# Kernel optimization log

Measured on AMD Instinct MI355X. Metric: run time of the kernel, lower is better.

The kernel has to match this reference:

```python
import jax, jax.numpy as jnp
import numpy as np

H, DR, DN = 16, 64, 64
HD = DR + DN  # 128
EPS = 1e-6


def _ln(t):
    m = t.mean(-1, keepdims=True)
    v = ((t - m) ** 2).mean(-1, keepdims=True)
    return (t - m) / jnp.sqrt(v + EPS)


def _rms(t, w):
    return t * jax.lax.rsqrt((t * t).mean(-1, keepdims=True) + EPS) * w


def _rot(t, fcs):
    # t: [b,s,h,DR]; fcs: [s, DR//2, 2] (cos,sin); complex multiply on pairs
    b, s, h, d = t.shape
    tr = t.reshape(b, s, h, d // 2, 2)
    x0, x1 = tr[..., 0], tr[..., 1]
    cos = fcs[None, :, None, :, 0]
    sin = fcs[None, :, None, :, 1]
    o0 = x0 * cos - x1 * sin
    o1 = x0 * sin + x1 * cos
    return jnp.stack([o0, o1], axis=-1).reshape(b, s, h, d)


def setup_inputs() -> dict:
    key = jax.random.key(0)
    ks = jax.random.split(key, 12)
    B, SX, SY, D = 1, 2048, 512, 2048
    s = 0.02
    pos_x = jnp.arange(SX, dtype=jnp.float32)
    pos_y = jnp.arange(SY, dtype=jnp.float32)
    inv = 1.0 / (10000.0 ** (jnp.arange(0, DR, 2, dtype=jnp.float32) / DR))  # [32]
    ang_x = pos_x[:, None] * inv[None, :]
    ang_y = pos_y[:, None] * inv[None, :]
    return {
        "x": jax.random.normal(ks[0], (B, SX, D), jnp.float32),
        "y": jax.random.normal(ks[1], (B, SY, D), jnp.float32),
        "mod": jax.random.normal(ks[2], (B, D), jnp.float32),
        "freqs_x": jnp.stack([jnp.cos(ang_x), jnp.sin(ang_x)], -1),
        "freqs_y": jnp.stack([jnp.cos(ang_y), jnp.sin(ang_y)], -1),
        "mask_x": jnp.ones((B, SX), bool),
        "mask_y": jnp.ones((B, SY), bool),
        "Wqkv_x": jax.random.normal(ks[3], (HD * H * 3, D), jnp.float32) * s,
        "bqkv_x": jnp.zeros((HD * H * 3,), jnp.float32),
        "Wqkv_y": jax.random.normal(ks[4], (HD * H * 3, D), jnp.float32) * s,
        "bqkv_y": jnp.zeros((HD * H * 3,), jnp.float32),
        "Wout": jax.random.normal(ks[5], (D, HD * H), jnp.float32) * s,
        "bout": jnp.zeros((D,), jnp.float32),
        "wq": jnp.ones((HD,), jnp.float32),
        "wk": jnp.ones((HD,), jnp.float32),
        "Wmod_q": jax.random.normal(ks[6], (D * 3, D), jnp.float32) * s,
        "bmod_q": jnp.zeros((D * 3,), jnp.float32),
        "Wmod_kv": jax.random.normal(ks[7], (D * 3, D), jnp.float32) * s,
        "bmod_kv": jnp.zeros((D * 3,), jnp.float32),
    }


def reference(x, y, mod, freqs_x, freqs_y, mask_x, mask_y, Wqkv_x, bqkv_x,
              Wqkv_y, bqkv_y, Wout, bout, wq, wk, Wmod_q, bmod_q, Wmod_kv, bmod_kv):
    b, sx, D = x.shape
    sy = y.shape[1]
    sz = sx + sy
    x_res, y_res = x, y
    xn = _ln(x)
    yn = _ln(y)
    # modulation from mod vector [b, D] -> [b, 1, 3D]
    mq = mod[:, None, :] @ Wmod_q.T + bmod_q
    bias_x, scale_x, gate_x = jnp.split(mq, 3, axis=-1)
    mkv = mod[:, None, :] @ Wmod_kv.T + bmod_kv
    bias_y, scale_y, gate_y = jnp.split(mkv, 3, axis=-1)
    xm = (1.0 + scale_x) * xn + bias_x
    ym = (1.0 + scale_y) * yn + bias_y
    qx, kx, vx = jnp.split(xm @ Wqkv_x.T + bqkv_x, 3, axis=-1)
    qy, ky, vy = jnp.split(ym @ Wqkv_y.T + bqkv_y, 3, axis=-1)
    q = jnp.concatenate([qx, qy], 1).reshape(b, sz, H, HD)
    k = jnp.concatenate([kx, ky], 1).reshape(b, sz, H, HD)
    v = jnp.concatenate([vx, vy], 1).reshape(b, sz, H, HD)
    q = _rms(q, wq)
    k = _rms(k, wk)
    q_rope, q_nope = q[..., :DR], q[..., DR:]
    k_rope, k_nope = k[..., :DR], k[..., DR:]
    fxx = jnp.concatenate([freqs_x, jnp.zeros_like(freqs_y)], 0)
    fyy = jnp.concatenate([jnp.zeros_like(freqs_x), freqs_y], 0)
    qf = jnp.concatenate([_rot(q_rope, fxx), _rot(q_rope, fyy), q_nope], -1)
    kf = jnp.concatenate([_rot(k_rope, fxx), _rot(k_rope, fyy), k_nope], -1)
    d_attn = 2 * DR + DN  # 192
    scale = 1.0 / jnp.sqrt(jnp.float32(d_attn))
    scores = jnp.einsum('bshd,bthd->bhst', qf, kf) * scale
    mask = jnp.concatenate([mask_x, mask_y], 1)  # [b, sz] bool, key-side
    scores = jnp.where(mask[:, None, None, :], scores, -jnp.inf)
    attn = jax.nn.softmax(scores, axis=-1)
    z = jnp.einsum('bhst,bthd->bshd', attn, v).reshape(b, sz, H * HD)
    z = z @ Wout.T + bout
    xo = z[:, :sx] * gate_x + x_res
    yo = z[:, sx:] * gate_y + y_res
    return jnp.concatenate([xo, yo], axis=1)  # [b, sz, D]
```

## Files before the change

### kernel.cpp

```cpp
#include <hip/hip_runtime.h>
#include <math.h>

#define H_    16
#define DR_   64
#define HD_   128
#define D_    2048
#define SX_   2048
#define SY_   512
#define SZ_   2560
#define NQKV_ 6144
#define EPS_  1e-6f
#define ATTN_SCALE 0.07216878364870323f
#define NS_   4
#define SPL_  (SZ_ / NS_)
#define QT_   (SZ_ / 128)

typedef __attribute__((ext_vector_type(8)))  short short8;
typedef __attribute__((ext_vector_type(16))) float f32x16;

__device__ __forceinline__ unsigned short f2bf(float f) {
    unsigned u = __builtin_bit_cast(unsigned, f);
    u += 0x7FFF + ((u >> 16) & 1);
    return (unsigned short)(u >> 16);
}
__device__ __forceinline__ unsigned pack2(float a, float b) {
    return (unsigned)f2bf(a) | ((unsigned)f2bf(b) << 16);
}
__device__ __forceinline__ float bf2f_lo(unsigned u) {
    return __builtin_bit_cast(float, u << 16);
}
__device__ __forceinline__ float bf2f_hi(unsigned u) {
    return __builtin_bit_cast(float, u & 0xffff0000u);
}

__device__ __forceinline__ unsigned cvtpk_bf16(float lo, float hi) {
    unsigned r;
    asm volatile("v_cvt_pk_bf16_f32 %0, %1, %2" : "=v"(r) : "v"(lo), "v"(hi));
    return r;
}

__device__ __forceinline__ void gload16(const unsigned short* g, unsigned short* l) {
    __builtin_amdgcn_global_load_lds(
        (const __attribute__((address_space(1))) unsigned*)g,
        (__attribute__((address_space(3))) unsigned*)l, 16, 0, 0);
}

__device__ __forceinline__ int xcd_swz(int hw, int nwg) {
    return (hw & 7) * (nwg >> 3) + (hw >> 3);
}

__device__ __forceinline__ short8 mkfrag(const float* p) {
    unsigned a01 = cvtpk_bf16(p[0], p[1]);
    unsigned a23 = cvtpk_bf16(p[2], p[3]);
    unsigned a45 = cvtpk_bf16(p[4], p[5]);
    unsigned a67 = cvtpk_bf16(p[6], p[7]);
    asm volatile("v_permlane32_swap_b32 %0, %1" : "+v"(a01), "+v"(a45));
    asm volatile("v_permlane32_swap_b32 %0, %1" : "+v"(a23), "+v"(a67));
    union { unsigned u[4]; short8 s; } r;
    r.u[0] = a01; r.u[1] = a23; r.u[2] = a45; r.u[3] = a67;
    return r.s;
}

__global__ __launch_bounds__(256) void cvt_all_kernel(
    const float* __restrict__ s1, const float* __restrict__ s2, const float* __restrict__ s3,
    unsigned short* __restrict__ dst, int n1, int n2, int n3)
{
    int i = (blockIdx.x * 256 + threadIdx.x) * 8;
    if (i >= n1 + n2 + n3) return;
    const float* src;
    if (i < n1)            src = s1 + i;
    else if (i < n1 + n2)  src = s2 + (i - n1);
    else                   src = s3 + (i - n1 - n2);
    float4 a = *(const float4*)(src);
    float4 b = *(const float4*)(src + 4);
    uint4 pk;
    pk.x = pack2(a.x, a.y); pk.y = pack2(a.z, a.w);
    pk.z = pack2(b.x, b.y); pk.w = pack2(b.z, b.w);
    *(uint4*)(dst + i) = pk;
}

__global__ __launch_bounds__(256) void mod_gemv_kernel(
    const float* __restrict__ mod,
    const float* __restrict__ Wq, const float* __restrict__ bq,
    const float* __restrict__ Wkv, const float* __restrict__ bkv,
    float* __restrict__ mq, float* __restrict__ mkv)
{
    int t = threadIdx.x;
    int row = blockIdx.x * 4 + (t >> 6);
    int lane = t & 63;
    const float* W; const float* b; float* out; int r;
    if (row < NQKV_) { W = Wq;  b = bq;  out = mq;  r = row; }
    else             { W = Wkv; b = bkv; out = mkv; r = row - NQKV_; }
    const float* wr = W + (size_t)r * D_;
    float s = 0.f;
    for (int k = lane; k < D_; k += 64) s += wr[k] * mod[k];
#pragma unroll
    for (int m = 32; m >= 1; m >>= 1) s += __shfl_xor(s, m);
    if (lane == 0) out[r] = s + b[r];
}

__global__ __launch_bounds__(256) void ln_mod_kernel(
    const float* __restrict__ x, const float* __restrict__ y,
    const float* __restrict__ mq, const float* __restrict__ mkv,
    unsigned short* __restrict__ xm)
{
    __shared__ float red[8];
    int s = blockIdx.x, t = threadIdx.x;
    const float* src; const float* mv;
    if (s < SX_) { src = x + (size_t)s * D_;          mv = mq; }
    else         { src = y + (size_t)(s - SX_) * D_;  mv = mkv; }
    float a[8];
    *(float4*)&a[0] = *(const float4*)(src + t * 8);
    *(float4*)&a[4] = *(const float4*)(src + t * 8 + 4);
    float sum = 0.f, ssq = 0.f;
#pragma unroll
    for (int i = 0; i < 8; ++i) { sum += a[i]; ssq += a[i] * a[i]; }
#pragma unroll
    for (int m = 32; m >= 1; m >>= 1) { sum += __shfl_xor(sum, m); ssq += __shfl_xor(ssq, m); }
    if ((t & 63) == 0) { red[t >> 6] = sum; red[4 + (t >> 6)] = ssq; }
    __syncthreads();
    float tot  = red[0] + red[1] + red[2] + red[3];
    float totq = red[4] + red[5] + red[6] + red[7];
    float mean = tot * (1.f / (float)D_);
    float var  = totq * (1.f / (float)D_) - mean * mean;
    float inv  = rsqrtf(var + EPS_);
    float o[8];
#pragma unroll
    for (int i = 0; i < 8; ++i) {
        int c = t * 8 + i;
        float v = (a[i] - mean) * inv;
        o[i] = (1.f + mv[D_ + c]) * v + mv[c];
    }
    uint4 pk;
    pk.x = pack2(o[0], o[1]); pk.y = pack2(o[2], o[3]);
    pk.z = pack2(o[4], o[5]); pk.w = pack2(o[6], o[7]);
    *(uint4*)(xm + (size_t)s * D_ + t * 8) = pk;
}

__global__ __launch_bounds__(256) void gemm_bf16_kernel(
    const unsigned short* __restrict__ A,
    const unsigned short* __restrict__ Wx, const float* __restrict__ bx,
    const unsigned short* __restrict__ Wy, const float* __restrict__ by,
    void* __restrict__ Cout, int N,
    const float* __restrict__ gx, const float* __restrict__ gy,
    const float* __restrict__ rx, const float* __restrict__ ry,
    int mode)
{
    __shared__ __align__(16) unsigned short As[2][128 * 32];
    __shared__ __align__(16) unsigned short Bs[2][128 * 32];
    int m0 = blockIdx.y * 128, n0 = blockIdx.x * 128;
    const unsigned short* W = (m0 < SX_) ? Wx : Wy;
    const float* bb = (m0 < SX_) ? bx : by;
    int t = threadIdx.x;
    int wv = t >> 6, lane = t & 63, l31 = lane & 31, g = lane >> 5;
    int wr = wv >> 1, wc = wv & 1;
    int srow = t >> 2, ssl = t & 3;
    const unsigned short* gA = A + (size_t)(m0 + srow) * D_ + ((ssl ^ ((srow >> 1) & 3)) * 8);
    const unsigned short* gW = W + (size_t)(n0 + srow) * D_ + ((ssl ^ ((srow >> 1) & 3)) * 8);
    f32x16 acc[2][2];
#pragma unroll
    for (int i = 0; i < 2; ++i)
#pragma unroll
        for (int j = 0; j < 2; ++j)
#pragma unroll
            for (int r = 0; r < 16; ++r) acc[i][j][r] = 0.f;
    int arow = wr * 64 + l31;
    int wrow = wc * 64 + l31;
    int a3 = (arow >> 1) & 3, w3 = (wrow >> 1) & 3;

    gload16(gA,            &As[0][wv * 512]);
    gload16(gA + 64 * D_,  &As[0][2048 + wv * 512]);
    gload16(gW,            &Bs[0][wv * 512]);
    gload16(gW + 64 * D_,  &Bs[0][2048 + wv * 512]);
    __syncthreads();

    for (int k0 = 0; k0 < D_; k0 += 32) {
        int cur = (k0 >> 5) & 1;
        if (k0 + 32 < D_) {
            int nb = cur ^ 1;
            gload16(gA + k0 + 32,           &As[nb][wv * 512]);
            gload16(gA + 64 * D_ + k0 + 32, &As[nb][2048 + wv * 512]);
            gload16(gW + k0 + 32,           &Bs[nb][wv * 512]);
            gload16(gW + 64 * D_ + k0 + 32, &Bs[nb][2048 + wv * 512]);
        }
#pragma unroll
        for (int kk = 0; kk < 2; ++kk) {
            int slot = kk * 2 + g;
            short8 af[2], wf[2];
#pragma unroll
            for (int i = 0; i < 2; ++i) {
                af[i] = *(const short8*)&As[cur][(arow + i * 32) * 32 + ((slot ^ a3) * 8)];
                wf[i] = *(const short8*)&Bs[cur][(wrow + i * 32) * 32 + ((slot ^ w3) * 8)];
            }
#pragma unroll
            for (int i = 0; i < 2; ++i)
#pragma unroll
                for (int j = 0; j < 2; ++j)
                    acc[i][j] = __builtin_amdgcn_mfma_f32_32x32x16_bf16(wf[j], af[i], acc[i][j], 0, 0, 0);
        }
        __syncthreads();
    }

#pragma unroll
    for (int i = 0; i < 2; ++i) {
        int row = m0 + wr * 64 + i * 32 + l31;
        if (mode == 0) {
            unsigned short* C = (unsigned short*)Cout;
#pragma unroll
            for (int j = 0; j < 2; ++j)
#pragma unroll
                for (int q = 0; q < 4; ++q) {
                    int n = n0 + wc * 64 + j * 32 + q * 8 + 4 * g;
                    float o0 = acc[i][j][q * 4 + 0] + bb[n + 0];
                    float o1 = acc[i][j][q * 4 + 1] + bb[n + 1];
                    float o2 = acc[i][j][q * 4 + 2] + bb[n + 2];
                    float o3 = acc[i][j][q * 4 + 3] + bb[n + 3];
                    *(uint2*)(C + (size_t)row * N + n) = make_uint2(pack2(o0, o1), pack2(o2, o3));
                }
        } else {
            float* C = (float*)Cout;
            const float* gt = (row < SX_) ? gx : gy;
            const float* rr = (row < SX_) ? rx + (size_t)row * N : ry + (size_t)(row - SX_) * N;
#pragma unroll
            for (int j = 0; j < 2; ++j)
#pragma unroll
                for (int q = 0; q < 4; ++q) {
                    int n = n0 + wc * 64 + j * 32 + q * 8 + 4 * g;
                    float4 o;
                    o.x = (acc[i][j][q * 4 + 0] + bb[n + 0]) * gt[n + 0] + rr[n + 0];
                    o.y = (acc[i][j][q * 4 + 1] + bb[n + 1]) * gt[n + 1] + rr[n + 1];
                    o.z = (acc[i][j][q * 4 + 2] + bb[n + 2]) * gt[n + 2] + rr[n + 2];
                    o.w = (acc[i][j][q * 4 + 3] + bb[n + 3]) * gt[n + 3] + rr[n + 3];
                    *(float4*)(C + (size_t)row * N + n) = o;
                }
        }
    }
}

__global__ __launch_bounds__(256) void qkv_transform_kernel(
    const unsigned short* __restrict__ qkv,
    const float* __restrict__ fx, const float* __restrict__ fy,
    const float* __restrict__ wq, const float* __restrict__ wk,
    unsigned short* __restrict__ qh, unsigned short* __restrict__ kh,
    unsigned short* __restrict__ vh)
{
    int t = threadIdx.x;
    int gid = blockIdx.x * 4 + (t >> 6);
    int lane = t & 63;
    int s = gid >> 4;
    int h = gid & 15;
    const unsigned short* base = qkv + (size_t)s * NQKV_ + h * HD_;
    int d = lane * 2;
    unsigned qu = *(const unsigned*)(base + d);
    unsigned ku = *(const unsigned*)(base + 2048 + d);
    unsigned vu = *(const unsigned*)(base + 4096 + d);
    float qx = bf2f_lo(qu), qy = bf2f_hi(qu);
    float kx = bf2f_lo(ku), ky = bf2f_hi(ku);
    float sq = qx * qx + qy * qy;
    float sk = kx * kx + ky * ky;
#pragma unroll
    for (int m = 32; m >= 1; m >>= 1) { sq += __shfl_xor(sq, m); sk += __shfl_xor(sk, m); }
    float qs = rsqrtf(sq * (1.f / 128.f) + EPS_) * ATTN_SCALE;
    float ks = rsqrtf(sk * (1.f / 128.f) + EPS_);
    float q0 = qx * qs * wq[d], q1 = qy * qs * wq[d + 1];
    float k0 = kx * ks * wk[d], k1 = ky * ks * wk[d + 1];
    if (lane < 32) {
        const float* f = (s < SX_) ? fx + (size_t)s * DR_ + d
                                   : fy + (size_t)(s - SX_) * DR_ + d;
        float cs = f[0], sn = f[1];
        float o0 = q0 * cs - q1 * sn, o1 = q0 * sn + q1 * cs;
        q0 = o0; q1 = o1;
        o0 = k0 * cs - k1 * sn; o1 = k0 * sn + k1 * cs;
        k0 = o0; k1 = o1;
    }
    size_t off = ((size_t)h * SZ_ + s) * HD_ + d;
    *(unsigned*)(qh + off) = pack2(q0, q1);
    *(unsigned*)(kh + off) = pack2(k0, k1);
    *(unsigned*)(vh + off) = vu;
}

__global__ __launch_bounds__(256) void vtrans_kernel(
    const unsigned short* __restrict__ vh, unsigned short* __restrict__ vt)
{
    __shared__ __align__(16) unsigned short T[64][72];
    int h = blockIdx.z, d0 = blockIdx.y * 64, s0 = blockIdx.x * 64;
    int t = threadIdx.x;
    int r = t >> 2, c = (t & 3) * 16;
    const unsigned short* src = vh + ((size_t)h * SZ_ + s0 + r) * HD_ + d0 + c;
    *(short8*)&T[r][c]     = *(const short8*)(src);
    *(short8*)&T[r][c + 8] = *(const short8*)(src + 8);
    __syncthreads();
    unsigned short o16[16];
#pragma unroll
    for (int i = 0; i < 16; ++i) o16[i] = T[c + i][r];
    unsigned short* dst = vt + ((size_t)h * HD_ + d0 + r) * SZ_ + s0 + c;
    *(short8*)dst       = *(short8*)&o16[0];
    *(short8*)(dst + 8) = *(short8*)&o16[8];
}

__global__ __launch_bounds__(256) void attn_mfma_kernel(
    const unsigned short* __restrict__ qh, const unsigned short* __restrict__ kh,
    const unsigned short* __restrict__ vt,
    unsigned short* __restrict__ Opart, float* __restrict__ mpart, float* __restrict__ lpart)
{
    __shared__ __align__(16) short Ks[2][64 * 128];
    __shared__ __align__(16) short Vs[2][128 * 64];
    int hw = (blockIdx.z * gridDim.y + blockIdx.y) * gridDim.x + blockIdx.x;
    int lg = xcd_swz(hw, QT_ * H_ * NS_);
    int qt    = lg % QT_;
    int hs    = lg / QT_;
    int h     = hs % H_;
    int split = hs / H_;
    int t = threadIdx.x;
    int wv = t >> 6, lane = t & 63;
    int l31 = lane & 31, g = lane >> 5;
    int bq = qt * 128 + wv * 32;
    const unsigned short* kbase = kh + (size_t)h * SZ_ * HD_;
    const unsigned short* vbase = vt + (size_t)h * HD_ * SZ_;

    int koff[4], voff[4];
#pragma unroll
    for (int i = 0; i < 4; ++i) {
        int idx = i * 256 + t;
        int r = idx >> 4, sl = idx & 15;
        koff[i] = r * HD_ + (((sl & 8) | ((sl ^ (r & 7)) & 7)) * 8);
        int r2 = idx >> 3, sl2 = idx & 7;
        voff[i] = r2 * SZ_ + ((sl2 ^ (r2 & 7)) * 8);
    }
    int ldsOff = wv * 512;

    short8 qf[8];
    {
        const unsigned short* qb = qh + ((size_t)h * SZ_ + bq + l31) * HD_ + g * 8;
#pragma unroll
        for (int s = 0; s < 8; ++s) qf[s] = *(const short8*)(qb + s * 16);
    }

    f32x16 o[4];
#pragma unroll
    for (int db = 0; db < 4; ++db)
#pragma unroll
        for (int r = 0; r < 16; ++r) o[db][r] = 0.f;
    float mreg = -INFINITY, lreg = 0.f;
    bool qY = (bq >= SX_);
    int sw7 = l31 & 7;
    int ts0 = split * SPL_;
    const int NT = SPL_ / 64;

#pragma unroll
    for (int i = 0; i < 4; ++i)
        gload16(kbase + (size_t)ts0 * HD_ + koff[i], (unsigned short*)&Ks[0][0] + i * 2048 + ldsOff);
#pragma unroll
    for (int i = 0; i < 4; ++i)
        gload16(vbase + ts0 + voff[i], (unsigned short*)&Vs[0][0] + i * 2048 + ldsOff);
    __syncthreads();

    for (int it = 0; it < NT; ++it) {
        int t0 = ts0 + it * 64;
        int cur = it & 1;
        if (it + 1 < NT) {
            int nb = cur ^ 1;
            const unsigned short* kn = kbase + (size_t)(t0 + 64) * HD_;
            const unsigned short* vn = vbase + (t0 + 64);
#pragma unroll
            for (int i = 0; i < 4; ++i)
                gload16(kn + koff[i], (unsigned short*)&Ks[nb][0] + i * 2048 + ldsOff);
#pragma unroll
            for (int i = 0; i < 4; ++i)
                gload16(vn + voff[i], (unsigned short*)&Vs[nb][0] + i * 2048 + ldsOff);
        }

        bool same = (qY == (t0 >= SX_));
        f32x16 sc0, sc1;
#pragma unroll
        for (int r = 0; r < 16; ++r) { sc0[r] = 0.f; sc1[r] = 0.f; }
        const short* Krow0 = &Ks[cur][0] + l31 * 128;
        const short* Krow1 = &Ks[cur][0] + (l31 + 32) * 128;
        __builtin_amdgcn_s_setprio(1);
#pragma unroll
        for (int s = 4; s < 8; ++s) {
            int slot = 2 * s + g;
            int sl = (slot & 8) | ((slot ^ sw7) & 7);
            sc0 = __builtin_amdgcn_mfma_f32_32x32x16_bf16(*(const short8*)(Krow0 + sl * 8), qf[s], sc0, 0, 0, 0);
            sc1 = __builtin_amdgcn_mfma_f32_32x32x16_bf16(*(const short8*)(Krow1 + sl * 8), qf[s], sc1, 0, 0, 0);
        }
        if (same) {
#pragma unroll
            for (int s = 0; s < 4; ++s) {
                int slot = 2 * s + g;
                int sl = (slot & 8) | ((slot ^ sw7) & 7);
                sc0 = __builtin_amdgcn_mfma_f32_32x32x16_bf16(*(const short8*)(Krow0 + sl * 8), qf[s], sc0, 0, 0, 0);
                sc1 = __builtin_amdgcn_mfma_f32_32x32x16_bf16(*(const short8*)(Krow1 + sl * 8), qf[s], sc1, 0, 0, 0);
            }
        }
        __builtin_amdgcn_s_setprio(0);

        float pm = -INFINITY;
#pragma unroll
        for (int r = 0; r < 16; ++r) pm = fmaxf(pm, fmaxf(sc0[r], sc1[r]));
        pm = fmaxf(pm, __shfl_xor(pm, 32));
        float mnew = fmaxf(mreg, pm);
        float corr = __expf(mreg - mnew);
        mreg = mnew;
        float pp0[16], pp1[16]; float rs = 0.f;
#pragma unroll
        for (int r = 0; r < 16; ++r) {
            pp0[r] = __expf(sc0[r] - mnew);
            pp1[r] = __expf(sc1[r] - mnew);
            rs += pp0[r] + pp1[r];
        }
        rs += __shfl_xor(rs, 32);
        lreg = lreg * corr + rs;
#pragma unroll
        for (int db = 0; db < 4; ++db)
#pragma unroll
            for (int r = 0; r < 16; ++r) o[db][r] *= corr;

        short8 pa0 = mkfrag(&pp0[0]), pa1 = mkfrag(&pp0[8]);
        short8 pa2 = mkfrag(&pp1[0]), pa3 = mkfrag(&pp1[8]);
        const short* Vb = &Vs[cur][0];
        __builtin_amdgcn_s_setprio(1);
#pragma unroll
        for (int ks = 0; ks < 4; ++ks) {
            short8 pf = (ks == 0) ? pa0 : (ks == 1) ? pa1 : (ks == 2) ? pa2 : pa3;
#pragma unroll
            for (int db = 0; db < 4; ++db) {
                int row = db * 32 + l31;
                int sl = (2 * ks + g) ^ (l31 & 7);
                const short8 vf = *(const short8*)(Vb + row * 64 + sl * 8);
                o[db] = __builtin_amdgcn_mfma_f32_32x32x16_bf16(vf, pf, o[db], 0, 0, 0);
            }
        }
        __builtin_amdgcn_s_setprio(0);
        __syncthreads();
    }

    int basep = ((split * QT_ + qt) * H_ + h) * 128 + wv * 32 + l31;
    unsigned short* op = Opart + (size_t)basep * 128;
#pragma unroll
    for (int db = 0; db < 4; ++db)
#pragma unroll
        for (int r = 0; r < 16; ++r) {
            int d = db * 32 + (r & 3) + 8 * (r >> 2) + 4 * g;
            op[d] = f2bf(o[db][r]);
        }
    if (g == 0) { mpart[basep] = mreg; lpart[basep] = lreg; }
}

__global__ __launch_bounds__(256) void attn_combine_kernel(
    const unsigned short* __restrict__ Opart,
    const float* __restrict__ mpart, const float* __restrict__ lpart,
    unsigned short* __restrict__ z)
{
    int t = threadIdx.x;
    int gid = blockIdx.x * 4 + (t >> 6);
    int lane = t & 63;
    int h = gid & 15;
    int r = gid >> 4;
    int qtile = r >> 7, qi = r & 127;
    int pidx[NS_];
    float m[NS_];
    float mx = -INFINITY;
#pragma unroll
    for (int s = 0; s < NS_; ++s) {
        pidx[s] = ((s * QT_ + qtile) * H_ + h) * 128 + qi;
        m[s] = mpart[pidx[s]];
        mx = fmaxf(mx, m[s]);
    }
    float L = 0.f;
    float w[NS_];
#pragma unroll
    for (int s = 0; s < NS_; ++s) {
        w[s] = __expf(m[s] - mx);
        L += w[s] * lpart[pidx[s]];
    }
    float invL = 1.f / L;
    int d = lane * 2;
    float a0 = 0.f, a1 = 0.f;
#pragma unroll
    for (int s = 0; s < NS_; ++s) {
        unsigned u = *(const unsigned*)(Opart + (size_t)pidx[s] * 128 + d);
        a0 += w[s] * bf2f_lo(u);
        a1 += w[s] * bf2f_hi(u);
    }
    *(unsigned*)(z + (size_t)r * D_ + h * HD_ + d) = pack2(a0 * invL, a1 * invL);
}

extern "C" void kernel_launch(void* const* d_in, const int* in_sizes, int n_in,
                              void* d_out, int out_size, void* d_ws, size_t ws_size,
                              hipStream_t stream) {
    const float* x    = (const float*)d_in[0];
    const float* y    = (const float*)d_in[1];
    const float* mod  = (const float*)d_in[2];
    const float* fx   = (const float*)d_in[3];
    const float* fy   = (const float*)d_in[4];
    const float* Wqx  = (const float*)d_in[7];
    const float* bqx  = (const float*)d_in[8];
    const float* Wqy  = (const float*)d_in[9];
    const float* bqy  = (const float*)d_in[10];
    const float* Wout = (const float*)d_in[11];
    const float* bout = (const float*)d_in[12];
    const float* wq   = (const float*)d_in[13];
    const float* wk   = (const float*)d_in[14];
    const float* Wmq  = (const float*)d_in[15];
    const float* bmq  = (const float*)d_in[16];
    const float* Wmk  = (const float*)d_in[17];
    const float* bmk  = (const float*)d_in[18];

    float* mq   = (float*)d_ws;
    float* mkv  = mq + NQKV_;
    unsigned short* xm   = (unsigned short*)(mkv + NQKV_);
    unsigned short* qkvb = xm + (size_t)SZ_ * D_;
    unsigned short* qh   = qkvb + (size_t)SZ_ * NQKV_;
    unsigned short* kh   = qh + (size_t)H_ * SZ_ * HD_;
    unsigned short* vh   = kh + (size_t)H_ * SZ_ * HD_;
    unsigned short* vt   = vh + (size_t)H_ * SZ_ * HD_;
    unsigned short* wqxb = vt + (size_t)H_ * SZ_ * HD_;
    unsigned short* wqyb = wqxb + (size_t)NQKV_ * D_;
    unsigned short* wob  = wqyb + (size_t)NQKV_ * D_;
    unsigned short* z    = xm;
    unsigned short* Opart = wqxb;
    float* mpart = (float*)qkvb;
    float* lpart = mpart + NS_ * QT_ * H_ * 128;
    float* out  = (float*)d_out;

    const int n1 = NQKV_ * D_, n3 = D_ * D_;
    hipLaunchKernelGGL(cvt_all_kernel, dim3((2 * n1 + n3) / 2048), dim3(256), 0, stream,
                       Wqx, Wqy, Wout, wqxb, n1, n1, n3);
    hipLaunchKernelGGL(mod_gemv_kernel, dim3(2 * NQKV_ / 4), dim3(256), 0, stream,
                       mod, Wmq, bmq, Wmk, bmk, mq, mkv);
    hipLaunchKernelGGL(ln_mod_kernel, dim3(SZ_), dim3(256), 0, stream,
                       x, y, mq, mkv, xm);
    hipLaunchKernelGGL(gemm_bf16_kernel, dim3(NQKV_ / 128, SZ_ / 128), dim3(256), 0, stream,
                       xm, wqxb, bqx, wqyb, bqy, (void*)qkvb, NQKV_,
                       (const float*)nullptr, (const float*)nullptr,
                       (const float*)nullptr, (const float*)nullptr, 0);
    hipLaunchKernelGGL(qkv_transform_kernel, dim3(SZ_ * H_ / 4), dim3(256), 0, stream,
                       qkvb, fx, fy, wq, wk, qh, kh, vh);
    hipLaunchKernelGGL(vtrans_kernel, dim3(SZ_ / 64, HD_ / 64, H_), dim3(256), 0, stream,
                       vh, vt);
    hipLaunchKernelGGL(attn_mfma_kernel, dim3(QT_, H_, NS_), dim3(256), 0, stream,
                       qh, kh, vt, Opart, mpart, lpart);
    hipLaunchKernelGGL(attn_combine_kernel, dim3(SZ_ * H_ / 4), dim3(256), 0, stream,
                       Opart, mpart, lpart, z);
    hipLaunchKernelGGL(gemm_bf16_kernel, dim3(D_ / 128, SZ_ / 128), dim3(256), 0, stream,
                       z, wob, bout, wob, bout, (void*)out, D_,
                       mq + 2 * D_, mkv + 2 * D_, x, y, 1);
}
```

Before: 343.8 us.

## Deepen GEMM pipeline to two k-stages per barrier; read V directly from QKV buffer

The bf16 GEMM now uses four LDS buffers and processes two 32-wide k-slices per iteration. It loads the next pair while computing the current pair, with a single vmcnt wait and barrier per 64 k. This halves the number of barriers and gives the loads more time to overlap with MFMA work, at the cost of doubling LDS use per block, which may lower occupancy. Separately, the V head-major intermediate copy is removed and the transpose kernel reads V straight from the QKV GEMM output, saving one write and one read pass.

```diff
diff --git a/kernel.cpp b/kernel.cpp
--- a/kernel.cpp
+++ b/kernel.cpp
@@ -146,8 +146,8 @@
     const float* __restrict__ rx, const float* __restrict__ ry,
     int mode)
 {
-    __shared__ __align__(16) unsigned short As[2][128 * 32];
-    __shared__ __align__(16) unsigned short Bs[2][128 * 32];
+    __shared__ __align__(16) unsigned short As[4][128 * 32];
+    __shared__ __align__(16) unsigned short Bs[4][128 * 32];
     int m0 = blockIdx.y * 128, n0 = blockIdx.x * 128;
     const unsigned short* W = (m0 < SX_) ? Wx : Wy;
     const float* bb = (m0 < SX_) ? bx : by;
@@ -168,37 +168,49 @@
     int wrow = wc * 64 + l31;
     int a3 = (arow >> 1) & 3, w3 = (wrow >> 1) & 3;
 
-    gload16(gA,            &As[0][wv * 512]);
-    gload16(gA + 64 * D_,  &As[0][2048 + wv * 512]);
-    gload16(gW,            &Bs[0][wv * 512]);
-    gload16(gW + 64 * D_,  &Bs[0][2048 + wv * 512]);
-    __syncthreads();
-
-    for (int k0 = 0; k0 < D_; k0 += 32) {
-        int cur = (k0 >> 5) & 1;
-        if (k0 + 32 < D_) {
-            int nb = cur ^ 1;
-            gload16(gA + k0 + 32,           &As[nb][wv * 512]);
-            gload16(gA + 64 * D_ + k0 + 32, &As[nb][2048 + wv * 512]);
-            gload16(gW + k0 + 32,           &Bs[nb][wv * 512]);
-            gload16(gW + 64 * D_ + k0 + 32, &Bs[nb][2048 + wv * 512]);
-        }
-#pragma unroll
-        for (int kk = 0; kk < 2; ++kk) {
-            int slot = kk * 2 + g;
-            short8 af[2], wf[2];
-#pragma unroll
-            for (int i = 0; i < 2; ++i) {
-                af[i] = *(const short8*)&As[cur][(arow + i * 32) * 32 + ((slot ^ a3) * 8)];
-                wf[i] = *(const short8*)&Bs[cur][(wrow + i * 32) * 32 + ((slot ^ w3) * 8)];
+#pragma unroll
+    for (int s = 0; s < 2; ++s) {
+        gload16(gA + s * 32,           &As[s][wv * 512]);
+        gload16(gA + 64 * D_ + s * 32, &As[s][2048 + wv * 512]);
+        gload16(gW + s * 32,           &Bs[s][wv * 512]);
+        gload16(gW + 64 * D_ + s * 32, &Bs[s][2048 + wv * 512]);
+    }
+
+    const int NIT = D_ / 64;
+    for (int it = 0; it < NIT; ++it) {
+        int rb = (it & 1) * 2;
+        asm volatile("s_waitcnt vmcnt(0)" ::: "memory");
+        __builtin_amdgcn_s_barrier();
+        if (it + 1 < NIT) {
+            int k2 = (2 * it + 2) * 32;
+            int pb = 2 - rb;
+#pragma unroll
+            for (int s = 0; s < 2; ++s) {
+                gload16(gA + k2 + s * 32,           &As[pb + s][wv * 512]);
+                gload16(gA + 64 * D_ + k2 + s * 32, &As[pb + s][2048 + wv * 512]);
+                gload16(gW + k2 + s * 32,           &Bs[pb + s][wv * 512]);
+                gload16(gW + 64 * D_ + k2 + s * 32, &Bs[pb + s][2048 + wv * 512]);
             }
-#pragma unroll
-            for (int i = 0; i < 2; ++i)
-#pragma unroll
-                for (int j = 0; j < 2; ++j)
-                    acc[i][j] = __builtin_amdgcn_mfma_f32_32x32x16_bf16(wf[j], af[i], acc[i][j], 0, 0, 0);
-        }
-        __syncthreads();
+        }
+#pragma unroll
+        for (int s = 0; s < 2; ++s) {
+            int cur = rb + s;
+#pragma unroll
+            for (int kk = 0; kk < 2; ++kk) {
+                int slot = kk * 2 + g;
+                short8 af[2], wf[2];
+#pragma unroll
+                for (int i = 0; i < 2; ++i) {
+                    af[i] = *(const short8*)&As[cur][(arow + i * 32) * 32 + ((slot ^ a3) * 8)];
+                    wf[i] = *(const short8*)&Bs[cur][(wrow + i * 32) * 32 + ((slot ^ w3) * 8)];
+                }
+#pragma unroll
+                for (int i = 0; i < 2; ++i)
+#pragma unroll
+                    for (int j = 0; j < 2; ++j)
+                        acc[i][j] = __builtin_amdgcn_mfma_f32_32x32x16_bf16(wf[j], af[i], acc[i][j], 0, 0, 0);
+            }
+        }
     }
 
 #pragma unroll
@@ -241,8 +253,7 @@
     const unsigned short* __restrict__ qkv,
     const float* __restrict__ fx, const float* __restrict__ fy,
     const float* __restrict__ wq, const float* __restrict__ wk,
-    unsigned short* __restrict__ qh, unsigned short* __restrict__ kh,
-    unsigned short* __restrict__ vh)
+    unsigned short* __restrict__ qh, unsigned short* __restrict__ kh)
 {
     int t = threadIdx.x;
     int gid = blockIdx.x * 4 + (t >> 6);
@@ -253,7 +264,6 @@
     int d = lane * 2;
     unsigned qu = *(const unsigned*)(base + d);
     unsigned ku = *(const unsigned*)(base + 2048 + d);
-    unsigned vu = *(const unsigned*)(base + 4096 + d);
     float qx = bf2f_lo(qu), qy = bf2f_hi(qu);
     float kx = bf2f_lo(ku), ky = bf2f_hi(ku);
     float sq = qx * qx + qy * qy;
@@ -276,17 +286,16 @@
     size_t off = ((size_t)h * SZ_ + s) * HD_ + d;
     *(unsigned*)(qh + off) = pack2(q0, q1);
     *(unsigned*)(kh + off) = pack2(k0, k1);
-    *(unsigned*)(vh + off) = vu;
 }
 
 __global__ __launch_bounds__(256) void vtrans_kernel(
-    const unsigned short* __restrict__ vh, unsigned short* __restrict__ vt)
+    const unsigned short* __restrict__ qkvb, unsigned short* __restrict__ vt)
 {
     __shared__ __align__(16) unsigned short T[64][72];
     int h = blockIdx.z, d0 = blockIdx.y * 64, s0 = blockIdx.x * 64;
     int t = threadIdx.x;
     int r = t >> 2, c = (t & 3) * 16;
-    const unsigned short* src = vh + ((size_t)h * SZ_ + s0 + r) * HD_ + d0 + c;
+    const unsigned short* src = qkvb + (size_t)(s0 + r) * NQKV_ + 4096 + h * HD_ + d0 + c;
     *(short8*)&T[r][c]     = *(const short8*)(src);
     *(short8*)&T[r][c + 8] = *(const short8*)(src + 8);
     __syncthreads();
@@ -536,9 +545,9 @@
                        (const float*)nullptr, (const float*)nullptr,
                        (const float*)nullptr, (const float*)nullptr, 0);
     hipLaunchKernelGGL(qkv_transform_kernel, dim3(SZ_ * H_ / 4), dim3(256), 0, stream,
-                       qkvb, fx, fy, wq, wk, qh, kh, vh);
+                       qkvb, fx, fy, wq, wk, qh, kh);
     hipLaunchKernelGGL(vtrans_kernel, dim3(SZ_ / 64, HD_ / 64, H_), dim3(256), 0, stream,
-                       vh, vt);
+                       qkvb, vt);
     hipLaunchKernelGGL(attn_mfma_kernel, dim3(QT_, H_, NS_), dim3(256), 0, stream,
                        qh, kh, vt, Opart, mpart, lpart);
     hipLaunchKernelGGL(attn_combine_kernel, dim3(SZ_ * H_ / 4), dim3(256), 0, stream,
```

After: 344.6 us. About the same (+0.2%).
